# Performance work log

Measured on AMD Instinct MI355X. Metric: run time of the kernel, lower is better.

The kernel has to match this reference:

```python
import jax, jax.numpy as jnp
import numpy as np

NUM_EXPERTS = 8
TOP_K = 2


def setup_inputs() -> dict:
    key = jax.random.key(0)
    ks = jax.random.split(key, 8)
    B = 16384
    D = 1024
    feat0 = jax.random.normal(ks[0], (B, 768), dtype=jnp.float32)
    feat1 = jax.random.normal(ks[1], (B, 512), dtype=jnp.float32)
    feat2 = jax.random.normal(ks[2], (B, 256), dtype=jnp.float32)
    # parameters (scaled like torch default init ~1/sqrt(fan_in))
    W_shared = jax.random.normal(ks[3], (1536, D), dtype=jnp.float32) * (1.0 / np.sqrt(1536))
    b_shared = jnp.zeros((D,), dtype=jnp.float32)
    W_gate = jax.random.normal(ks[4], (D, NUM_EXPERTS), dtype=jnp.float32) * (1.0 / np.sqrt(D))
    b_gate = jnp.zeros((NUM_EXPERTS,), dtype=jnp.float32)
    W_experts = jax.random.normal(ks[5], (NUM_EXPERTS, D, D), dtype=jnp.float32) * (1.0 / np.sqrt(D))
    b_experts = jnp.zeros((NUM_EXPERTS, D), dtype=jnp.float32)
    return {
        "feat0": feat0, "feat1": feat1, "feat2": feat2,
        "W_shared": W_shared, "b_shared": b_shared,
        "W_gate": W_gate, "b_gate": b_gate,
        "W_experts": W_experts, "b_experts": b_experts,
    }


def _moe_forward(feat0, feat1, feat2, W_shared, b_shared, W_gate, b_gate, W_experts, b_experts):
    x = jnp.concatenate([feat0, feat1, feat2], axis=1)          # (B, sum_d)
    h = jax.nn.gelu(x @ W_shared + b_shared, approximate=False)  # (B, D)
    gate_probs = jax.nn.softmax(h @ W_gate + b_gate, axis=-1)    # (B, E)
    topk_probs, topk_idx = jax.lax.top_k(gate_probs, TOP_K)      # (B, K)
    out = jnp.zeros_like(h)
    for e in range(NUM_EXPERTS):
        # per-token combine weight for expert e (0 if not routed to e)
        w_e = jnp.sum(topk_probs * (topk_idx == e), axis=1)      # (B,)
        expert_out = jax.nn.gelu(h @ W_experts[e] + b_experts[e], approximate=False)
        out = out + w_e[:, None] * expert_out
    return out


def reference(feat0, feat1, feat2, W_shared, b_shared, W_gate, b_gate, W_experts, b_experts):
    return _moe_forward(feat0, feat1, feat2, W_shared, b_shared, W_gate, b_gate, W_experts, b_experts)
```

## Files before the change

kernel.cpp:

```cpp
#include <hip/hip_runtime.h>
#include <math.h>

#define NB_TOK 16384
#define DM     1024
#define NEXP   8
#define KIN    1536
#define SECBIT 0x40000000
#define TOKMSK 0x3FFFFFFF

typedef __attribute__((ext_vector_type(8))) short          short8;
typedef __attribute__((ext_vector_type(8))) unsigned short ushort8;
typedef __attribute__((ext_vector_type(4))) unsigned short ushort4v;
typedef __attribute__((ext_vector_type(8))) _Float16       half8;
typedef __attribute__((ext_vector_type(4))) float          floatx4;

#define AS1U(p) ((const __attribute__((address_space(1))) unsigned int*)(p))
#define AS3U(p) ((__attribute__((address_space(3))) unsigned int*)(p))

__device__ __forceinline__ float gelu_f(float x) {
    const float ax = fabsf(x) * 0.70710678118654752440f;
    const float t  = 1.0f / fmaf(0.3275911f, ax, 1.0f);
    float p = fmaf(t, 1.061405429f, -1.453152027f);
    p = fmaf(t, p, 1.421413741f);
    p = fmaf(t, p, -0.284496736f);
    p = fmaf(t, p, 0.254829592f);
    p = p * t;
    const float e = __expf(-ax * ax);
    float erf = fmaf(-p, e, 1.0f);
    erf = copysignf(erf, x);
    return 0.5f * x * (1.0f + erf);
}

__device__ __forceinline__ unsigned short f2bf(float x) {
    unsigned u = __float_as_uint(x);
    u = (u + 0x7FFF + ((u >> 16) & 1)) >> 16;
    return (unsigned short)u;
}

__device__ __forceinline__ void split_h16(float x, unsigned short& hi, unsigned short& lo) {
    _Float16 h = (_Float16)x;
    float r = x - (float)h;
    _Float16 l = (_Float16)r;
    hi = *(unsigned short*)&h;
    lo = *(unsigned short*)&l;
}

__global__ __launch_bounds__(256) void k_splitA(
    const float* __restrict__ f0, const float* __restrict__ f1,
    const float* __restrict__ f2, unsigned short* __restrict__ Ah,
    unsigned short* __restrict__ Al)
{
    const int i4  = blockIdx.x * 256 + threadIdx.x;
    const int tok = i4 / (KIN / 4);
    const int k   = (i4 % (KIN / 4)) * 4;
    const float* src; int ld, c;
    if (k < 768)       { src = f0; ld = 768; c = k; }
    else if (k < 1280) { src = f1; ld = 512; c = k - 768; }
    else               { src = f2; ld = 256; c = k - 1280; }
    const float4 v = *(const float4*)(src + (size_t)tok * ld + c);
    const float* vp = (const float*)&v;
    ushort4v hi, lo;
#pragma unroll
    for (int j = 0; j < 4; ++j) {
        unsigned short h, l;
        split_h16(vp[j] * 4.0f, h, l);
        hi[j] = h; lo[j] = l;
    }
    *(ushort4v*)(Ah + (size_t)tok * KIN + k) = hi;
    *(ushort4v*)(Al + (size_t)tok * KIN + k) = lo;
}

__global__ __launch_bounds__(256) void k_splitB(
    const float* __restrict__ Ws, unsigned short* __restrict__ BhT,
    unsigned short* __restrict__ BlT)
{
    __shared__ float s[32][33];
    const int n0 = blockIdx.x * 32, k0 = blockIdx.y * 32;
    const int c  = threadIdx.x & 31, r = threadIdx.x >> 5;
#pragma unroll
    for (int p = 0; p < 4; ++p)
        s[r + p * 8][c] = Ws[(size_t)(k0 + r + p * 8) * DM + n0 + c];
    __syncthreads();
#pragma unroll
    for (int p = 0; p < 4; ++p) {
        const int n = r + p * 8;
        unsigned short h, l;
        split_h16(s[c][n] * 256.0f, h, l);
        BhT[(size_t)(n0 + n) * KIN + k0 + c] = h;
        BlT[(size_t)(n0 + n) * KIN + k0 + c] = l;
    }
}

__global__ __launch_bounds__(512) void k_shared_mfma(
    const unsigned short* __restrict__ Ah, const unsigned short* __restrict__ Al,
    const unsigned short* __restrict__ BhT, const unsigned short* __restrict__ BlT,
    const float* __restrict__ bs, float* __restrict__ h)
{
    __shared__ unsigned short ldsAh[128][64];
    __shared__ unsigned short ldsAl[128][64];
    __shared__ unsigned short ldsBh[128][64];
    __shared__ unsigned short ldsBl[128][64];

    const int t    = threadIdx.x;
    const int lane = t & 63;
    const int wave = t >> 6;
    const int bid  = blockIdx.x;
    const int brow = ((bid >> 6) << 3) + (bid & 7);
    const int bcol = (bid >> 3) & 7;
    const int row0 = brow * 128;
    const int n0g  = bcol * 128;

    const int srow = t >> 3;
    const int g    = (t & 7) ^ (srow & 7);
    const unsigned short *sAh[2], *sAl[2], *sBh[2], *sBl[2];
#pragma unroll
    for (int q = 0; q < 2; ++q) {
        const size_t ra = (size_t)(row0 + q * 64 + srow) * KIN + g * 8;
        const size_t rb = (size_t)(n0g + q * 64 + srow) * KIN + g * 8;
        sAh[q] = Ah + ra; sAl[q] = Al + ra;
        sBh[q] = BhT + rb; sBl[q] = BlT + rb;
    }

    const int grp = lane >> 4;
    const int wr = wave >> 2, wc = wave & 3;
    int offA[2][4], offB[2][2];
#pragma unroll
    for (int ks = 0; ks < 2; ++ks) {
#pragma unroll
        for (int m = 0; m < 4; ++m) {
            const int rA = wr * 64 + m * 16 + (lane & 15);
            const int c  = ks * 4 + grp;
            offA[ks][m] = rA * 128 + (((c ^ (rA & 7)) & 7) << 4);
        }
#pragma unroll
        for (int n = 0; n < 2; ++n) {
            const int rB = wc * 32 + n * 16 + (lane & 15);
            const int c  = ks * 4 + grp;
            offB[ks][n] = rB * 128 + (((c ^ (rB & 7)) & 7) << 4);
        }
    }

    floatx4 acc[4][2];
#pragma unroll
    for (int m = 0; m < 4; ++m)
#pragma unroll
        for (int n = 0; n < 2; ++n) acc[m][n] = (floatx4){0.f, 0.f, 0.f, 0.f};

    const char* lAh = (const char*)&ldsAh[0][0];
    const char* lAl = (const char*)&ldsAl[0][0];
    const char* lBh = (const char*)&ldsBh[0][0];
    const char* lBl = (const char*)&ldsBl[0][0];

    for (int kt = 0; kt < KIN / 64; ++kt) {
        const int k0 = kt * 64;
        __syncthreads();
#pragma unroll
        for (int q = 0; q < 2; ++q) {
            const int dst = q * 8192 + t * 16;
            __builtin_amdgcn_global_load_lds(AS1U(sAh[q] + k0), AS3U((char*)lAh + dst), 16, 0, 0);
            __builtin_amdgcn_global_load_lds(AS1U(sAl[q] + k0), AS3U((char*)lAl + dst), 16, 0, 0);
            __builtin_amdgcn_global_load_lds(AS1U(sBh[q] + k0), AS3U((char*)lBh + dst), 16, 0, 0);
            __builtin_amdgcn_global_load_lds(AS1U(sBl[q] + k0), AS3U((char*)lBl + dst), 16, 0, 0);
        }
        __syncthreads();
#pragma unroll
        for (int ks = 0; ks < 2; ++ks) {
            half8 ah[4], al[4], bh[2], bl[2];
#pragma unroll
            for (int m = 0; m < 4; ++m) {
                ah[m] = *(const half8*)(lAh + offA[ks][m]);
                al[m] = *(const half8*)(lAl + offA[ks][m]);
            }
#pragma unroll
            for (int n = 0; n < 2; ++n) {
                bh[n] = *(const half8*)(lBh + offB[ks][n]);
                bl[n] = *(const half8*)(lBl + offB[ks][n]);
            }
#pragma unroll
            for (int m = 0; m < 4; ++m)
#pragma unroll
                for (int n = 0; n < 2; ++n) {
                    acc[m][n] = __builtin_amdgcn_mfma_f32_16x16x32_f16(ah[m], bh[n], acc[m][n], 0, 0, 0);
                    acc[m][n] = __builtin_amdgcn_mfma_f32_16x16x32_f16(ah[m], bl[n], acc[m][n], 0, 0, 0);
                    acc[m][n] = __builtin_amdgcn_mfma_f32_16x16x32_f16(al[m], bh[n], acc[m][n], 0, 0, 0);
                }
        }
    }

#pragma unroll
    for (int n = 0; n < 2; ++n) {
        const int col  = n0g + wc * 32 + n * 16 + (lane & 15);
        const float bias = bs[col];
#pragma unroll
        for (int m = 0; m < 4; ++m) {
            const int rbase = row0 + wr * 64 + m * 16 + (lane >> 4) * 4;
#pragma unroll
            for (int reg = 0; reg < 4; ++reg) {
                const float o = gelu_f(acc[m][n][reg] * (1.0f / 1024.0f) + bias);
                h[(size_t)(rbase + reg) * DM + col] = o;
            }
        }
    }
}

__global__ __launch_bounds__(256) void k_wt_bf16(
    const float* __restrict__ We, unsigned short* __restrict__ WeT)
{
    __shared__ float s[32][33];
    const int e  = blockIdx.z;
    const int k0 = blockIdx.y * 32, n0 = blockIdx.x * 32;
    const int c  = threadIdx.x & 31, r = threadIdx.x >> 5;
    const float* W = We + ((size_t)e << 20);
#pragma unroll
    for (int p = 0; p < 4; ++p) {
        const int k = r + p * 8;
        s[k][c] = W[(size_t)(k0 + k) * DM + n0 + c];
    }
    __syncthreads();
#pragma unroll
    for (int p = 0; p < 4; ++p) {
        const int n = r + p * 8;
        WeT[((size_t)e << 20) + (size_t)(n0 + n) * DM + k0 + c] = f2bf(s[c][n]);
    }
}

__global__ __launch_bounds__(256) void k_gate_topk(
    const float* __restrict__ h, const float* __restrict__ Wg,
    const float* __restrict__ bg, int* __restrict__ eidx,
    float2* __restrict__ w01)
{
    const int lane = threadIdx.x & 63;
    const int wv   = threadIdx.x >> 6;
    const int tok  = blockIdx.x * 4 + wv;
    const float* hr = h + (size_t)tok * DM;
    float acc[NEXP];
#pragma unroll
    for (int e = 0; e < NEXP; ++e) acc[e] = 0.f;
    for (int j = 0; j < DM / 64; ++j) {
        const float hv = hr[lane + 64 * j];
        const float* wr = Wg + (size_t)(lane + 64 * j) * NEXP;
#pragma unroll
        for (int e = 0; e < NEXP; ++e) acc[e] = fmaf(hv, wr[e], acc[e]);
    }
#pragma unroll
    for (int off = 32; off > 0; off >>= 1) {
#pragma unroll
        for (int e = 0; e < NEXP; ++e) acc[e] += __shfl_xor(acc[e], off, 64);
    }
    if (lane == 0) {
        float lg[NEXP];
        float mx = -1e30f;
#pragma unroll
        for (int e = 0; e < NEXP; ++e) { lg[e] = acc[e] + bg[e]; mx = fmaxf(mx, lg[e]); }
        float p[NEXP]; float s = 0.f;
#pragma unroll
        for (int e = 0; e < NEXP; ++e) { p[e] = expf(lg[e] - mx); s += p[e]; }
        const float inv = 1.f / s;
        int i0 = 0;
#pragma unroll
        for (int e = 1; e < NEXP; ++e) if (p[e] > p[i0]) i0 = e;
        int i1 = (i0 == 0) ? 1 : 0;
#pragma unroll
        for (int e = 0; e < NEXP; ++e) if (e != i0 && p[e] > p[i1]) i1 = e;
        eidx[tok] = i0 | (i1 << 8);
        w01[tok]  = make_float2(p[i0] * inv, p[i1] * inv);
    }
}

__global__ __launch_bounds__(256) void k_bucket(
    const int* __restrict__ eidx,
    int* __restrict__ counts, int* __restrict__ btok)
{
    __shared__ int lcnt[NEXP], lbase[NEXP];
    const int tid = threadIdx.x;
    const int tok = blockIdx.x * 256 + tid;
    if (tid < NEXP) lcnt[tid] = 0;
    __syncthreads();
    const int ee = eidx[tok];
    const int e0 = ee & 0xff, e1 = ee >> 8;
    const int l0 = atomicAdd(&lcnt[e0], 1);
    const int l1 = atomicAdd(&lcnt[e1], 1);
    __syncthreads();
    if (tid < NEXP) lbase[tid] = atomicAdd(&counts[tid], lcnt[tid]);
    __syncthreads();
    btok[e0 * NB_TOK + lbase[e0] + l0] = tok;
    btok[e1 * NB_TOK + lbase[e1] + l1] = tok | SECBIT;
}

__global__ __launch_bounds__(256) void k_gather(
    const float* __restrict__ h, const int* __restrict__ btok,
    const int* __restrict__ counts, unsigned short* __restrict__ hbfc)
{
    const int g = blockIdx.x;
    int e = 0, base = 0, r = 0;
#pragma unroll
    for (int i = 0; i < NEXP; ++i) {
        if (g >= r) { e = i; base = r; }
        r += counts[i];
    }
    const int idx = g - base;
    const int tok = btok[e * NB_TOK + idx] & TOKMSK;
    const int c   = threadIdx.x * 4;
    const float4 v = *(const float4*)(h + (size_t)tok * DM + c);
    ushort4v o;
    o[0] = f2bf(v.x); o[1] = f2bf(v.y); o[2] = f2bf(v.z); o[3] = f2bf(v.w);
    *(ushort4v*)(hbfc + (size_t)g * DM + c) = o;
}

#define EXP_STAGE(k0)                                                                                 \
    {                                                                                                 \
        char* lAw = (char*)&ldsA[0][0];                                                               \
        char* lBw = (char*)&ldsB[0][0];                                                               \
        _Pragma("unroll")                                                                             \
        for (int q = 0; q < 4; ++q) {                                                                 \
            __builtin_amdgcn_global_load_lds(AS1U(srcA[q] + (k0)), AS3U(lAw + q * 4096 + wave * 1024), 16, 0, 0); \
            __builtin_amdgcn_global_load_lds(AS1U(srcB[q] + (k0)), AS3U(lBw + q * 4096 + wave * 1024), 16, 0, 0); \
        }                                                                                             \
    }

__global__ __launch_bounds__(256) void k_expert_mfma(
    const unsigned short* __restrict__ hbfc,
    const unsigned short* __restrict__ WeT,
    const float* __restrict__ bexp,
    const int* __restrict__ counts,
    const int* __restrict__ btok,
    float* __restrict__ stage2, float* __restrict__ out)
{
    const int bid = blockIdx.x;
    const int x   = bid & 7;
    const int nt  = (bid >> 3) & 7;
    const int gs  = bid >> 6;
    const int e   = (x + gs) & 7;
    const int rb  = gs;
    int gb = 0, cnt = 0, r_ = 0;
#pragma unroll
    for (int i = 0; i < NEXP; ++i) {
        if (i == e) { gb = r_; cnt = counts[i]; }
        r_ += counts[i];
    }
    const int row0 = rb * 128;
    if (row0 >= cnt) return;

    __shared__ unsigned short ldsA[128][64];
    __shared__ unsigned short ldsB[128][64];
    __shared__ int sTok[128];

    const int t    = threadIdx.x;
    const int lane = t & 63;
    const int wave = t >> 6;

    const int srow = t >> 3;
    const int g    = (t & 7) ^ (srow & 7);
    const int n0g  = nt * 128;
    const unsigned short* srcA[4];
    const unsigned short* srcB[4];
#pragma unroll
    for (int q = 0; q < 4; ++q) {
        srcA[q] = hbfc + (size_t)(gb + row0 + q * 32 + srow) * DM + g * 8;
        srcB[q] = WeT + ((size_t)e << 20) + (size_t)(n0g + q * 32 + srow) * DM + g * 8;
    }

    EXP_STAGE(0);

    if (t < 128) {
        const int idx = row0 + t;
        sTok[t] = (idx < cnt) ? btok[e * NB_TOK + idx] : 0;
    }

    const int grp = lane >> 4;
    int offA[2][4], offB[2][4];
#pragma unroll
    for (int ks = 0; ks < 2; ++ks)
#pragma unroll
        for (int m = 0; m < 4; ++m) {
            const int rA = ((wave >> 1) * 64) + m * 16 + (lane & 15);
            const int rB = ((wave & 1) * 64) + m * 16 + (lane & 15);
            const int c  = ks * 4 + grp;
            offA[ks][m] = rA * 128 + (((c ^ (rA & 7)) & 7) << 4);
            offB[ks][m] = rB * 128 + (((c ^ (rB & 7)) & 7) << 4);
        }

    floatx4 acc[4][4];
#pragma unroll
    for (int m = 0; m < 4; ++m)
#pragma unroll
        for (int n = 0; n < 4; ++n) acc[m][n] = (floatx4){0.f, 0.f, 0.f, 0.f};

    const char* lA = (const char*)&ldsA[0][0];
    const char* lB = (const char*)&ldsB[0][0];

    for (int kt = 0; kt < DM / 64; ++kt) {
        __syncthreads();
#pragma unroll
        for (int ks = 0; ks < 2; ++ks) {
            short8 av[4], bv[4];
#pragma unroll
            for (int m = 0; m < 4; ++m) av[m] = *(const short8*)(lA + offA[ks][m]);
#pragma unroll
            for (int n = 0; n < 4; ++n) bv[n] = *(const short8*)(lB + offB[ks][n]);
#pragma unroll
            for (int m = 0; m < 4; ++m)
#pragma unroll
                for (int n = 0; n < 4; ++n)
                    acc[m][n] = __builtin_amdgcn_mfma_f32_16x16x32_bf16(av[m], bv[n], acc[m][n], 0, 0, 0);
        }
        if (kt + 1 < DM / 64) {
            __syncthreads();
            EXP_STAGE((kt + 1) * 64);
        }
    }

    const int wr = wave >> 1, wc = wave & 1;
#pragma unroll
    for (int n = 0; n < 4; ++n) {
        const int col  = n0g + wc * 64 + n * 16 + (lane & 15);
        const float bias = bexp[e * DM + col];
#pragma unroll
        for (int m = 0; m < 4; ++m) {
            const int rbase = wr * 64 + m * 16 + (lane >> 4) * 4;
#pragma unroll
            for (int reg = 0; reg < 4; ++reg) {
                const int r = rbase + reg;
                if (row0 + r >= cnt) continue;
                const int raw = sTok[r];
                const int tok = raw & TOKMSK;
                float* dst = (raw & SECBIT) ? stage2 : out;
                dst[(size_t)tok * DM + col] = acc[m][n][reg] + bias;
            }
        }
    }
}

__global__ __launch_bounds__(256) void k_combine(
    const float* __restrict__ stage2, const float2* __restrict__ w01,
    float* __restrict__ out)
{
    const int tok = blockIdx.x;
    const int c   = threadIdx.x * 4;
    const float2 w = w01[tok];
    const float4 a = *(const float4*)(out    + (size_t)tok * DM + c);
    const float4 b = *(const float4*)(stage2 + (size_t)tok * DM + c);
    float4 o;
    o.x = w.x * gelu_f(a.x) + w.y * gelu_f(b.x);
    o.y = w.x * gelu_f(a.y) + w.y * gelu_f(b.y);
    o.z = w.x * gelu_f(a.z) + w.y * gelu_f(b.z);
    o.w = w.x * gelu_f(a.w) + w.y * gelu_f(b.w);
    *(float4*)(out + (size_t)tok * DM + c) = o;
}

extern "C" void kernel_launch(void* const* d_in, const int* in_sizes, int n_in,
                              void* d_out, int out_size, void* d_ws, size_t ws_size,
                              hipStream_t stream)
{
    const float* f0 = (const float*)d_in[0];
    const float* f1 = (const float*)d_in[1];
    const float* f2 = (const float*)d_in[2];
    const float* Ws = (const float*)d_in[3];
    const float* bs = (const float*)d_in[4];
    const float* Wg = (const float*)d_in[5];
    const float* bg = (const float*)d_in[6];
    const float* We = (const float*)d_in[7];
    const float* be = (const float*)d_in[8];
    float* out = (float*)d_out;

    const size_t MB = 1048576ULL;
    char* base = (char*)d_ws;
    unsigned short* Ah    = (unsigned short*)(base);
    unsigned short* Al    = (unsigned short*)(base + 48 * MB);
    unsigned short* BhT   = (unsigned short*)(base + 96 * MB);
    unsigned short* BlT   = (unsigned short*)(base + 99 * MB);
    float*          h     = (float*)(base + 102 * MB);
    unsigned short* WeT   = (unsigned short*)(base + 2 * MB);
    unsigned short* hbfc  = (unsigned short*)(base + 18 * MB);
    float*          stage2= (float*)(base + 82 * MB);
    int*    counts = (int*)(base);
    int*    btok   = counts + 64;
    int*    eidx   = (int*)(btok + NEXP * NB_TOK);
    float2* w01    = (float2*)(eidx + NB_TOK);

    k_splitA<<<NB_TOK * (KIN / 4) / 256, 256, 0, stream>>>(f0, f1, f2, Ah, Al);
    k_splitB<<<dim3(DM / 32, KIN / 32), 256, 0, stream>>>(Ws, BhT, BlT);
    k_shared_mfma<<<1024, 512, 0, stream>>>(Ah, Al, BhT, BlT, bs, h);

    hipMemsetAsync(counts, 0, 16 * sizeof(int), stream);
    k_gate_topk<<<NB_TOK / 4, 256, 0, stream>>>(h, Wg, bg, eidx, w01);
    k_bucket<<<NB_TOK / 256, 256, 0, stream>>>(eidx, counts, btok);
    k_gather<<<2 * NB_TOK, 256, 0, stream>>>(h, btok, counts, hbfc);

    k_wt_bf16<<<dim3(DM / 32, DM / 32, NEXP), 256, 0, stream>>>(We, WeT);

    k_expert_mfma<<<8192, 256, 0, stream>>>(
        hbfc, WeT, be, counts, btok, stage2, out);
    k_combine<<<NB_TOK, 256, 0, stream>>>(stage2, w01, out);
}
```

Baseline: 399.3 us.

## Fuse bf16 conversion into shared GEMM epilogue and gather tokens inside expert kernel

The shared GEMM epilogue now also writes a bf16 copy of h, and the separate gather kernel is removed. The expert GEMM loads token indices into LDS first and reads A rows indirectly from the dense bf16 h, so no compacted per-expert copy is needed. The gate kernel also switches to float4 loads of h. This removes a full read of h and the write and re-read of a compacted buffer, at the cost of extra bf16 stores in the GEMM epilogue, scattered row reads in the expert GEMM, and an added sync before the first stage.

```diff
diff --git a/kernel.cpp b/kernel.cpp
--- a/kernel.cpp
+++ b/kernel.cpp
@@ -94,7 +94,8 @@
 __global__ __launch_bounds__(512) void k_shared_mfma(
     const unsigned short* __restrict__ Ah, const unsigned short* __restrict__ Al,
     const unsigned short* __restrict__ BhT, const unsigned short* __restrict__ BlT,
-    const float* __restrict__ bs, float* __restrict__ h)
+    const float* __restrict__ bs, float* __restrict__ h,
+    unsigned short* __restrict__ hbf)
 {
     __shared__ unsigned short ldsAh[128][64];
     __shared__ unsigned short ldsAl[128][64];
@@ -103,7 +104,6 @@
 
     const int t    = threadIdx.x;
     const int lane = t & 63;
-    const int wave = t >> 6;
     const int bid  = blockIdx.x;
     const int brow = ((bid >> 6) << 3) + (bid & 7);
     const int bcol = (bid >> 3) & 7;
@@ -122,6 +122,7 @@
     }
 
     const int grp = lane >> 4;
+    const int wave = t >> 6;
     const int wr = wave >> 2, wc = wave & 3;
     int offA[2][4], offB[2][2];
 #pragma unroll
@@ -197,7 +198,8 @@
 #pragma unroll
             for (int reg = 0; reg < 4; ++reg) {
                 const float o = gelu_f(acc[m][n][reg] * (1.0f / 1024.0f) + bias);
-                h[(size_t)(rbase + reg) * DM + col] = o;
+                h[(size_t)(rbase + reg) * DM + col]   = o;
+                hbf[(size_t)(rbase + reg) * DM + col] = f2bf(o);
             }
         }
     }
@@ -236,11 +238,17 @@
     float acc[NEXP];
 #pragma unroll
     for (int e = 0; e < NEXP; ++e) acc[e] = 0.f;
-    for (int j = 0; j < DM / 64; ++j) {
-        const float hv = hr[lane + 64 * j];
-        const float* wr = Wg + (size_t)(lane + 64 * j) * NEXP;
-#pragma unroll
-        for (int e = 0; e < NEXP; ++e) acc[e] = fmaf(hv, wr[e], acc[e]);
+#pragma unroll
+    for (int j = 0; j < DM / 256; ++j) {
+        const int kb = lane * 4 + 256 * j;
+        const float4 hv = *(const float4*)(hr + kb);
+        const float* hvp = (const float*)&hv;
+#pragma unroll
+        for (int c = 0; c < 4; ++c) {
+            const float* wr = Wg + (size_t)(kb + c) * NEXP;
+#pragma unroll
+            for (int e = 0; e < NEXP; ++e) acc[e] = fmaf(hvp[c], wr[e], acc[e]);
+        }
     }
 #pragma unroll
     for (int off = 32; off > 0; off >>= 1) {
@@ -285,26 +293,6 @@
     __syncthreads();
     btok[e0 * NB_TOK + lbase[e0] + l0] = tok;
     btok[e1 * NB_TOK + lbase[e1] + l1] = tok | SECBIT;
-}
-
-__global__ __launch_bounds__(256) void k_gather(
-    const float* __restrict__ h, const int* __restrict__ btok,
-    const int* __restrict__ counts, unsigned short* __restrict__ hbfc)
-{
-    const int g = blockIdx.x;
-    int e = 0, base = 0, r = 0;
-#pragma unroll
-    for (int i = 0; i < NEXP; ++i) {
-        if (g >= r) { e = i; base = r; }
-        r += counts[i];
-    }
-    const int idx = g - base;
-    const int tok = btok[e * NB_TOK + idx] & TOKMSK;
-    const int c   = threadIdx.x * 4;
-    const float4 v = *(const float4*)(h + (size_t)tok * DM + c);
-    ushort4v o;
-    o[0] = f2bf(v.x); o[1] = f2bf(v.y); o[2] = f2bf(v.z); o[3] = f2bf(v.w);
-    *(ushort4v*)(hbfc + (size_t)g * DM + c) = o;
 }
 
 #define EXP_STAGE(k0)                                                                                 \
@@ -319,7 +307,7 @@
     }
 
 __global__ __launch_bounds__(256) void k_expert_mfma(
-    const unsigned short* __restrict__ hbfc,
+    const unsigned short* __restrict__ hbf,
     const unsigned short* __restrict__ WeT,
     const float* __restrict__ bexp,
     const int* __restrict__ counts,
@@ -332,12 +320,7 @@
     const int gs  = bid >> 6;
     const int e   = (x + gs) & 7;
     const int rb  = gs;
-    int gb = 0, cnt = 0, r_ = 0;
-#pragma unroll
-    for (int i = 0; i < NEXP; ++i) {
-        if (i == e) { gb = r_; cnt = counts[i]; }
-        r_ += counts[i];
-    }
+    const int cnt = counts[e];
     const int row0 = rb * 128;
     if (row0 >= cnt) return;
 
@@ -348,6 +331,12 @@
     const int t    = threadIdx.x;
     const int lane = t & 63;
     const int wave = t >> 6;
+
+    if (t < 128) {
+        const int idx = row0 + t;
+        sTok[t] = (idx < cnt) ? btok[e * NB_TOK + idx] : 0;
+    }
+    __syncthreads();
 
     const int srow = t >> 3;
     const int g    = (t & 7) ^ (srow & 7);
@@ -356,16 +345,12 @@
     const unsigned short* srcB[4];
 #pragma unroll
     for (int q = 0; q < 4; ++q) {
-        srcA[q] = hbfc + (size_t)(gb + row0 + q * 32 + srow) * DM + g * 8;
+        const int tk = sTok[q * 32 + srow] & TOKMSK;
+        srcA[q] = hbf + (size_t)tk * DM + g * 8;
         srcB[q] = WeT + ((size_t)e << 20) + (size_t)(n0g + q * 32 + srow) * DM + g * 8;
     }
 
     EXP_STAGE(0);
-
-    if (t < 128) {
-        const int idx = row0 + t;
-        sTok[t] = (idx < cnt) ? btok[e * NB_TOK + idx] : 0;
-    }
 
     const int grp = lane >> 4;
     int offA[2][4], offB[2][4];
@@ -470,8 +455,8 @@
     unsigned short* BhT   = (unsigned short*)(base + 96 * MB);
     unsigned short* BlT   = (unsigned short*)(base + 99 * MB);
     float*          h     = (float*)(base + 102 * MB);
+    unsigned short* hbf   = (unsigned short*)(base + 166 * MB);
     unsigned short* WeT   = (unsigned short*)(base + 2 * MB);
-    unsigned short* hbfc  = (unsigned short*)(base + 18 * MB);
     float*          stage2= (float*)(base + 82 * MB);
     int*    counts = (int*)(base);
     int*    btok   = counts + 64;
@@ -480,16 +465,15 @@
 
     k_splitA<<<NB_TOK * (KIN / 4) / 256, 256, 0, stream>>>(f0, f1, f2, Ah, Al);
     k_splitB<<<dim3(DM / 32, KIN / 32), 256, 0, stream>>>(Ws, BhT, BlT);
-    k_shared_mfma<<<1024, 512, 0, stream>>>(Ah, Al, BhT, BlT, bs, h);
+    k_shared_mfma<<<1024, 512, 0, stream>>>(Ah, Al, BhT, BlT, bs, h, hbf);
 
     hipMemsetAsync(counts, 0, 16 * sizeof(int), stream);
     k_gate_topk<<<NB_TOK / 4, 256, 0, stream>>>(h, Wg, bg, eidx, w01);
     k_bucket<<<NB_TOK / 256, 256, 0, stream>>>(eidx, counts, btok);
-    k_gather<<<2 * NB_TOK, 256, 0, stream>>>(h, btok, counts, hbfc);
 
     k_wt_bf16<<<dim3(DM / 32, DM / 32, NEXP), 256, 0, stream>>>(We, WeT);
 
     k_expert_mfma<<<8192, 256, 0, stream>>>(
-        hbfc, WeT, be, counts, btok, stage2, out);
+        hbf, WeT, be, counts, btok, stage2, out);
     k_combine<<<NB_TOK, 256, 0, stream>>>(stage2, w01, out);
 }
```

Result: slower. 428.7 us (+7.4%).
